# Kernel tuning notes

Measured on AMD Instinct MI355X. Metric: run time of the kernel, lower is better.

The kernel has to match this reference:

```python
import jax, jax.numpy as jnp
import numpy as np

NEG = -9e15  # kept for fidelity though mask is unused in original forward

def setup_inputs() -> dict:
    key = jax.random.key(0)
    k1, k2, k3 = jax.random.split(key, 3)
    N, Fin, Fout = 8192, 512, 256
    x = jax.random.normal(k1, (N, Fin), dtype=jnp.float32)
    # xavier_uniform with gain=1.414 ~ U(-b, b), b = gain*sqrt(6/(fan_in+fan_out))
    bW = 1.414 * np.sqrt(6.0 / (Fin + Fout))
    W = jax.random.uniform(k2, (Fin, Fout), minval=-bW, maxval=bW, dtype=jnp.float32)
    ba = 1.414 * np.sqrt(6.0 / (2 * Fout + 1))
    a = jax.random.uniform(k3, (2 * Fout, 1), minval=-ba, maxval=ba, dtype=jnp.float32)
    return {"x": x, "W": W, "a": a}

def reference(x, W, a):
    # h: [N, Fout]
    h = x @ W
    Fout = h.shape[1]
    # Algebraic decomposition of additive score: e_ij = relu(a1.h_i + a2.h_j)
    a1, a2 = a[:Fout, 0], a[Fout:, 0]  # [Fout], [Fout]
    f = h @ a1  # [N] contribution of row node i
    g = h @ a2  # [N] contribution of col node j
    e = jax.nn.relu(f[:, None] + g[None, :])  # [N, N]
    attention = jax.nn.softmax(e, axis=1)
    h_prime = attention @ h  # [N, Fout]
    return jax.nn.elu(h_prime)
```

## Files before the change

kernel.cpp:

```cpp
#include <hip/hip_runtime.h>
#include <math.h>

#define NROWS 8192
#define FIN   512
#define FOUT  256
#define NCHUNK 512
#define CHROWS 16

typedef _Float16 f16;
typedef _Float16 f16x8 __attribute__((ext_vector_type(8)));
typedef float    f32x4 __attribute__((ext_vector_type(4)));

__global__ __launch_bounds__(256) void prep(const float* __restrict__ x,
                                            const float* __restrict__ W,
                                            f16* __restrict__ xh,
                                            f16* __restrict__ Wt,
                                            float* __restrict__ fg) {
    const int b = blockIdx.x, t = threadIdx.x;
    if (b < 256) {
        const size_t base = (size_t)b * 16384;
#pragma unroll 4
        for (int i = 0; i < 16; ++i) {
            const size_t idx = base + (size_t)i * 1024 + t * 4;
            float4 v = *(const float4*)&x[idx];
            union { f16 h[4]; ushort4 u; } cv;
            cv.h[0] = (f16)v.x; cv.h[1] = (f16)v.y;
            cv.h[2] = (f16)v.z; cv.h[3] = (f16)v.w;
            *(ushort4*)&xh[idx] = cv.u;
        }
    } else {
        const int n = b - 256;
        Wt[(size_t)n * FIN + t]       = (f16)W[(size_t)t * FOUT + n];
        Wt[(size_t)n * FIN + t + 256] = (f16)W[(size_t)(t + 256) * FOUT + n];
        if (n < 64) fg[n * 256 + t] = 0.f;
    }
}

__global__ __launch_bounds__(256) void gemm_fg(const f16* __restrict__ xh,
                                               const f16* __restrict__ Wt,
                                               const float* __restrict__ a,
                                               f16* __restrict__ h,
                                               float* __restrict__ f,
                                               float* __restrict__ g) {
    __shared__ __align__(16) f16 As[64][136];
    __shared__ __align__(16) f16 Bs[64][136];
    __shared__ float sf[2][64], sg[2][64];
    const int tid = threadIdx.x;
    const int n0 = blockIdx.x * 64;
    const int m0 = blockIdx.y * 64;
    const int srow = tid >> 2, sseg = (tid & 3) * 8;
    const int w = tid >> 6, lane = tid & 63;
    const int wm = (w & 1) * 32, wn = (w >> 1) * 32;
    const int l15 = lane & 15, quad = lane >> 4;

    f16x8 pa[4], pb[4];
#pragma unroll
    for (int j = 0; j < 4; ++j) {
        pa[j] = *(const f16x8*)&xh[(size_t)(m0 + srow) * FIN + j * 32 + sseg];
        pb[j] = *(const f16x8*)&Wt[(size_t)(n0 + srow) * FIN + j * 32 + sseg];
    }

    f32x4 acc[2][2] = {};
    for (int k0 = 0; k0 < FIN; k0 += 128) {
        __syncthreads();
#pragma unroll
        for (int j = 0; j < 4; ++j) {
            *(f16x8*)&As[srow][j * 32 + sseg] = pa[j];
            *(f16x8*)&Bs[srow][j * 32 + sseg] = pb[j];
        }
        __syncthreads();
        if (k0 + 128 < FIN) {
#pragma unroll
            for (int j = 0; j < 4; ++j) {
                pa[j] = *(const f16x8*)&xh[(size_t)(m0 + srow) * FIN + k0 + 128 + j * 32 + sseg];
                pb[j] = *(const f16x8*)&Wt[(size_t)(n0 + srow) * FIN + k0 + 128 + j * 32 + sseg];
            }
        }
#pragma unroll
        for (int kk = 0; kk < 4; ++kk) {
            f16x8 af[2], bf[2];
#pragma unroll
            for (int ti = 0; ti < 2; ++ti)
                af[ti] = *(const f16x8*)&As[wm + ti * 16 + l15][kk * 32 + quad * 8];
#pragma unroll
            for (int tj = 0; tj < 2; ++tj)
                bf[tj] = *(const f16x8*)&Bs[wn + tj * 16 + l15][kk * 32 + quad * 8];
#pragma unroll
            for (int ti = 0; ti < 2; ++ti)
#pragma unroll
                for (int tj = 0; tj < 2; ++tj)
                    acc[ti][tj] = __builtin_amdgcn_mfma_f32_16x16x32_f16(af[ti], bf[tj], acc[ti][tj], 0, 0, 0);
        }
    }
#pragma unroll
    for (int ti = 0; ti < 2; ++ti)
#pragma unroll
        for (int tj = 0; tj < 2; ++tj) {
            const int col = n0 + wn + tj * 16 + l15;
#pragma unroll
            for (int r = 0; r < 4; ++r) {
                const int row = m0 + wm + ti * 16 + quad * 4 + r;
                h[(size_t)row * FOUT + col] = (f16)acc[ti][tj][r];
            }
        }
    const float a1c0 = a[n0 + wn + l15];
    const float a1c1 = a[n0 + wn + 16 + l15];
    const float a2c0 = a[FOUT + n0 + wn + l15];
    const float a2c1 = a[FOUT + n0 + wn + 16 + l15];
    const int wnIdx = w >> 1;
#pragma unroll
    for (int ti = 0; ti < 2; ++ti) {
        float pf[4], pg[4];
#pragma unroll
        for (int r = 0; r < 4; ++r) {
            pf[r] = acc[ti][0][r] * a1c0 + acc[ti][1][r] * a1c1;
            pg[r] = acc[ti][0][r] * a2c0 + acc[ti][1][r] * a2c1;
        }
#pragma unroll
        for (int off = 8; off >= 1; off >>= 1)
#pragma unroll
            for (int r = 0; r < 4; ++r) {
                pf[r] += __shfl_xor(pf[r], off, 16);
                pg[r] += __shfl_xor(pg[r], off, 16);
            }
        if (l15 == 0)
#pragma unroll
            for (int r = 0; r < 4; ++r) {
                sf[wnIdx][wm + ti * 16 + quad * 4 + r] = pf[r];
                sg[wnIdx][wm + ti * 16 + quad * 4 + r] = pg[r];
            }
    }
    __syncthreads();
    if (tid < 64) {
        atomicAdd(&f[m0 + tid], sf[0][tid] + sf[1][tid]);
        atomicAdd(&g[m0 + tid], sg[0][tid] + sg[1][tid]);
    }
}

__global__ __launch_bounds__(256) void rank_scatter(const float* __restrict__ g,
                                                    float* __restrict__ gs,
                                                    int* __restrict__ perm) {
    const int t = threadIdx.x;
    const int jl = t & 31;
    const int seg = t >> 5;
    const int j = blockIdx.x * 32 + jl;
    const float gj = g[j];
    const int base = seg * (NROWS / 8);
    int cnt = 0;
    for (int r = 0; r < NROWS / 8; r += 4) {
        const float4 v = *(const float4*)&g[base + r];
        const int i0 = base + r;
        cnt += (v.x < gj) || (v.x == gj && (i0 + 0) < j);
        cnt += (v.y < gj) || (v.y == gj && (i0 + 1) < j);
        cnt += (v.z < gj) || (v.z == gj && (i0 + 2) < j);
        cnt += (v.w < gj) || (v.w == gj && (i0 + 3) < j);
    }
    __shared__ int part[8][32];
    part[seg][jl] = cnt;
    __syncthreads();
    if (seg == 0) {
        int rank = 0;
#pragma unroll
        for (int s = 0; s < 8; ++s) rank += part[s][jl];
        gs[rank] = gj;
        perm[rank] = j;
    }
}

__global__ __launch_bounds__(256) void scan_pass1(const f16* __restrict__ h,
                                                  const int* __restrict__ perm,
                                                  const float* __restrict__ gs,
                                                  const float* __restrict__ f,
                                                  float* __restrict__ c0,
                                                  float* __restrict__ c1,
                                                  float* __restrict__ c1s,
                                                  int* __restrict__ n0arr) {
    const int b = blockIdx.x, c = threadIdx.x;
    if (b < NCHUNK) {
        const int base = b * CHROWS;
        __shared__ int p[CHROWS];
        __shared__ float wl[CHROWS];
        if (c < CHROWS) {
            p[c] = perm[base + c];
            wl[c] = expf(gs[base + c] - gs[NROWS - 1]);
        }
        __syncthreads();
        float s0 = 0.f, s1 = 0.f;
        for (int r = 0; r < CHROWS; ++r) {
            float v = (float)h[(size_t)p[r] * FOUT + c];
            s0 += v;
            s1 += wl[r] * v;
        }
        c0[b * FOUT + c] = s0;
        c1[b * FOUT + c] = s1;
        if (c == 0) {
            float t = 0.f;
            for (int r = 0; r < CHROWS; ++r) t += wl[r];
            c1s[b] = t;
        }
    } else {
        const int i = (b - NCHUNK) * 256 + c;
        const float tt = -f[i];
        int lo = 0, hi = NROWS;
        while (lo < hi) {
            int mid = (lo + hi) >> 1;
            if (gs[mid] <= tt) lo = mid + 1; else hi = mid;
        }
        n0arr[i] = lo;
    }
}

__global__ __launch_bounds__(256) void scan_pass2(const float* __restrict__ c0,
                                                  const float* __restrict__ c1,
                                                  const float* __restrict__ c1s,
                                                  float* __restrict__ o0,
                                                  float* __restrict__ o1,
                                                  float* __restrict__ o1s) {
    const int b = blockIdx.x, t = threadIdx.x;
    __shared__ float sb[256];
    if (b < 256) {
        const float e0 = c0[(2 * t) * FOUT + b];
        const float e1 = c0[(2 * t + 1) * FOUT + b];
        const float local = e0 + e1;
        sb[t] = local;
        __syncthreads();
        for (int off = 1; off < 256; off <<= 1) {
            float add = (t >= off) ? sb[t - off] : 0.f;
            __syncthreads();
            sb[t] += add;
            __syncthreads();
        }
        const float ex = sb[t] - local;
        o0[(2 * t) * FOUT + b] = ex;
        o0[(2 * t + 1) * FOUT + b] = ex + e0;
    } else if (b < 512) {
        const int col = b - 256;
        const float e0 = c1[(2 * t) * FOUT + col];
        const float e1 = c1[(2 * t + 1) * FOUT + col];
        const float local = e0 + e1;
        sb[t] = local;
        __syncthreads();
        for (int off = 1; off < 256; off <<= 1) {
            float add = (t + off < 256) ? sb[t + off] : 0.f;
            __syncthreads();
            sb[t] += add;
            __syncthreads();
        }
        const float exs = sb[t] - local;
        o1[(2 * t) * FOUT + col] = exs + e1;
        o1[(2 * t + 1) * FOUT + col] = exs;
    } else {
        const float e0 = c1s[2 * t];
        const float e1 = c1s[2 * t + 1];
        const float local = e0 + e1;
        sb[t] = local;
        __syncthreads();
        for (int off = 1; off < 256; off <<= 1) {
            float add = (t + off < 256) ? sb[t + off] : 0.f;
            __syncthreads();
            sb[t] += add;
            __syncthreads();
        }
        const float exs = sb[t] - local;
        o1s[2 * t] = exs + e1;
        o1s[2 * t + 1] = exs;
    }
}

__global__ __launch_bounds__(256) void scan_pass3(const f16* __restrict__ h,
                                                  const int* __restrict__ perm,
                                                  const float* __restrict__ gs,
                                                  const float* __restrict__ o0,
                                                  const float* __restrict__ o1,
                                                  const float* __restrict__ o1s,
                                                  f16* __restrict__ P0,
                                                  f16* __restrict__ S1,
                                                  float* __restrict__ S1s) {
    const int k = blockIdx.x, c = threadIdx.x;
    const int base = k * CHROWS;
    __shared__ int p[CHROWS];
    __shared__ float wl[CHROWS];
    if (c < CHROWS) {
        p[c] = perm[base + c];
        wl[c] = expf(gs[base + c] - gs[NROWS - 1]);
    }
    __syncthreads();
    float run0 = o0[k * FOUT + c];
    for (int r = 0; r < CHROWS; ++r) {
        P0[(size_t)(base + r) * FOUT + c] = (f16)run0;
        run0 += (float)h[(size_t)p[r] * FOUT + c];
    }
    float run1 = o1[k * FOUT + c];
    for (int r = CHROWS - 1; r >= 0; --r) {
        run1 += wl[r] * (float)h[(size_t)p[r] * FOUT + c];
        S1[(size_t)(base + r) * FOUT + c] = (f16)run1;
    }
    if (c == 0) {
        float rs = o1s[k];
        for (int r = CHROWS - 1; r >= 0; --r) { rs += wl[r]; S1s[base + r] = rs; }
    }
    if (k == NCHUNK - 1) {
        P0[(size_t)NROWS * FOUT + c] = (f16)run0;
        S1[(size_t)NROWS * FOUT + c] = (f16)0.f;
        if (c == 0) S1s[NROWS] = 0.f;
    }
}

__global__ __launch_bounds__(256) void final_kernel(const float* __restrict__ f,
                                                    const float* __restrict__ gs,
                                                    const int* __restrict__ n0arr,
                                                    const f16* __restrict__ P0,
                                                    const f16* __restrict__ S1,
                                                    const float* __restrict__ S1s,
                                                    float* __restrict__ out) {
    const int b = blockIdx.x, c = threadIdx.x;
    const float gm = gs[NROWS - 1];
#pragma unroll
    for (int rr = 0; rr < 4; ++rr) {
        const int i = b * 4 + rr;
        const float fi = f[i];
        const int n0 = n0arr[i];
        const float m = fmaxf(0.f, fi + gm);
        const float A = expf(-m);
        const float B = expf(fi + gm - m);
        const float denom = A * (float)n0 + B * S1s[n0];
        const float numer = A * (float)P0[(size_t)n0 * FOUT + c]
                          + B * (float)S1[(size_t)n0 * FOUT + c];
        const float v = numer / denom;
        out[(size_t)i * FOUT + c] = v > 0.f ? v : expm1f(v);
    }
}

extern "C" void kernel_launch(void* const* d_in, const int* in_sizes, int n_in,
                              void* d_out, int out_size, void* d_ws, size_t ws_size,
                              hipStream_t stream) {
    (void)in_sizes; (void)n_in; (void)out_size; (void)ws_size;
    const float* x = (const float*)d_in[0];
    const float* W = (const float*)d_in[1];
    const float* a = (const float*)d_in[2];
    float* out = (float*)d_out;

    char* ws = (char*)d_ws;
    size_t off = 0;
    auto alloc = [&](size_t bytes) -> void* {
        void* p = ws + off;
        off += (bytes + 255) & ~(size_t)255;
        return p;
    };
    f16*   xh   = (f16*)alloc((size_t)NROWS * FIN * 2);
    f16*   Wt   = (f16*)alloc((size_t)FOUT * FIN * 2);
    f16*   h    = (f16*)alloc((size_t)NROWS * FOUT * 2);
    f16*   P0   = (f16*)alloc((size_t)(NROWS + 1) * FOUT * 2);
    f16*   S1   = (f16*)alloc((size_t)(NROWS + 1) * FOUT * 2);
    float* fg   = (float*)alloc(2 * NROWS * 4);
    float* f    = fg;
    float* g    = fg + NROWS;
    float* gs   = (float*)alloc(NROWS * 4);
    int*   perm = (int*)alloc(NROWS * 4);
    int*   n0arr= (int*)alloc(NROWS * 4);
    float* c0   = (float*)alloc(NCHUNK * FOUT * 4);
    float* c1   = (float*)alloc(NCHUNK * FOUT * 4);
    float* o0   = (float*)alloc(NCHUNK * FOUT * 4);
    float* o1   = (float*)alloc(NCHUNK * FOUT * 4);
    float* c1s  = (float*)alloc(NCHUNK * 4);
    float* o1s  = (float*)alloc(NCHUNK * 4);
    float* S1s  = (float*)alloc((NROWS + 1) * 4);

    prep<<<512, 256, 0, stream>>>(x, W, xh, Wt, fg);
    gemm_fg<<<dim3(FOUT / 64, NROWS / 64), 256, 0, stream>>>(xh, Wt, a, h, f, g);
    rank_scatter<<<NROWS / 32, 256, 0, stream>>>(g, gs, perm);
    scan_pass1<<<NCHUNK + 32, 256, 0, stream>>>(h, perm, gs, f, c0, c1, c1s, n0arr);
    scan_pass2<<<513, 256, 0, stream>>>(c0, c1, c1s, o0, o1, o1s);
    scan_pass3<<<NCHUNK, 256, 0, stream>>>(h, perm, gs, o0, o1, o1s, P0, S1, S1s);
    final_kernel<<<NROWS / 4, 256, 0, stream>>>(f, gs, n0arr, P0, S1, S1s, out);
}
```

Measured before the change: 135.1 us.

## Fuse seven stage kernels into one persistent kernel with grid barriers

Replaces the seven separate launches (prep, GEMM, rank, three scan passes, final) with a single persistent kernel of 512 blocks that moves between stages through atomic-counter grid barriers. The counter is zeroed by a memset before launch. Each stage's work is remapped to 512 blocks: rank uses 16 columns per block and final handles 16 rows per block. The goal is to remove per-kernel launch gaps and tail effects. The cost is that all 512 blocks must be co-resident for the spin barriers to be safe, and each barrier adds global-atomic latency.

```diff
diff --git a/kernel.cpp b/kernel.cpp
--- a/kernel.cpp
+++ b/kernel.cpp
@@ -6,201 +6,302 @@
 #define FOUT  256
 #define NCHUNK 512
 #define CHROWS 16
+#define NB    512
 
 typedef _Float16 f16;
 typedef _Float16 f16x8 __attribute__((ext_vector_type(8)));
 typedef float    f32x4 __attribute__((ext_vector_type(4)));
 
-__global__ __launch_bounds__(256) void prep(const float* __restrict__ x,
-                                            const float* __restrict__ W,
-                                            f16* __restrict__ xh,
-                                            f16* __restrict__ Wt,
-                                            float* __restrict__ fg) {
-    const int b = blockIdx.x, t = threadIdx.x;
+constexpr size_t AL(size_t v) { return (v + 255) & ~(size_t)255; }
+constexpr size_t SZ_XH  = (size_t)NROWS * FIN * 2;
+constexpr size_t SZ_WT  = (size_t)FOUT * FIN * 2;
+constexpr size_t SZ_H   = (size_t)NROWS * FOUT * 2;
+constexpr size_t SZ_PS  = (size_t)(NROWS + 1) * FOUT * 2;
+constexpr size_t SZ_FG  = (size_t)2 * NROWS * 4;
+constexpr size_t SZ_I   = (size_t)NROWS * 4;
+constexpr size_t SZ_C   = (size_t)NCHUNK * FOUT * 4;
+constexpr size_t SZ_CS  = (size_t)NCHUNK * 4;
+constexpr size_t SZ_S1S = (size_t)(NROWS + 1) * 4;
+
+constexpr size_t OFF_XH   = 0;
+constexpr size_t OFF_WT   = OFF_XH   + AL(SZ_XH);
+constexpr size_t OFF_H    = OFF_WT   + AL(SZ_WT);
+constexpr size_t OFF_P0   = OFF_H    + AL(SZ_H);
+constexpr size_t OFF_S1   = OFF_P0   + AL(SZ_PS);
+constexpr size_t OFF_FG   = OFF_S1   + AL(SZ_PS);
+constexpr size_t OFF_GS   = OFF_FG   + AL(SZ_FG);
+constexpr size_t OFF_PERM = OFF_GS   + AL(SZ_I);
+constexpr size_t OFF_N0   = OFF_PERM + AL(SZ_I);
+constexpr size_t OFF_C0   = OFF_N0   + AL(SZ_I);
+constexpr size_t OFF_C1   = OFF_C0   + AL(SZ_C);
+constexpr size_t OFF_O0   = OFF_C1   + AL(SZ_C);
+constexpr size_t OFF_O1   = OFF_O0   + AL(SZ_C);
+constexpr size_t OFF_C1S  = OFF_O1   + AL(SZ_C);
+constexpr size_t OFF_O1S  = OFF_C1S  + AL(SZ_CS);
+constexpr size_t OFF_S1S  = OFF_O1S  + AL(SZ_CS);
+constexpr size_t OFF_CNT  = OFF_S1S  + AL(SZ_S1S);
+
+union SmemU {
+    struct { f16 As[64][136]; f16 Bs[64][136]; float sf[2][64], sg[2][64]; } g;
+    struct { int part[16][16]; } r;
+    struct { int p[CHROWS]; float wl[CHROWS]; } c;
+    struct { float sb[256]; } s;
+};
+
+__device__ __forceinline__ void gridbar(unsigned* cnt, unsigned target) {
+    __syncthreads();
+    if (threadIdx.x == 0) {
+        __hip_atomic_fetch_add(cnt, 1u, __ATOMIC_ACQ_REL, __HIP_MEMORY_SCOPE_AGENT);
+        while (__hip_atomic_load(cnt, __ATOMIC_ACQUIRE, __HIP_MEMORY_SCOPE_AGENT) < target) {
+        }
+    }
+    __syncthreads();
+}
+
+__global__ __launch_bounds__(256, 2) void mega(const float* __restrict__ x,
+                                               const float* __restrict__ W,
+                                               const float* __restrict__ a,
+                                               float* __restrict__ out,
+                                               char* __restrict__ ws) {
+    __shared__ SmemU sm;
+    const int b = blockIdx.x, tid = threadIdx.x;
+
+    f16*   xh   = (f16*)(ws + OFF_XH);
+    f16*   Wt   = (f16*)(ws + OFF_WT);
+    f16*   hb   = (f16*)(ws + OFF_H);
+    f16*   P0b  = (f16*)(ws + OFF_P0);
+    f16*   S1b  = (f16*)(ws + OFF_S1);
+    float* fArr = (float*)(ws + OFF_FG);
+    float* gArr = fArr + NROWS;
+    float* gs   = (float*)(ws + OFF_GS);
+    int*   perm = (int*)(ws + OFF_PERM);
+    int*   n0arr= (int*)(ws + OFF_N0);
+    float* c0   = (float*)(ws + OFF_C0);
+    float* c1   = (float*)(ws + OFF_C1);
+    float* o0   = (float*)(ws + OFF_O0);
+    float* o1   = (float*)(ws + OFF_O1);
+    float* c1s  = (float*)(ws + OFF_C1S);
+    float* o1s  = (float*)(ws + OFF_O1S);
+    float* S1s  = (float*)(ws + OFF_S1S);
+    unsigned* cnt = (unsigned*)(ws + OFF_CNT);
+
     if (b < 256) {
         const size_t base = (size_t)b * 16384;
 #pragma unroll 4
         for (int i = 0; i < 16; ++i) {
-            const size_t idx = base + (size_t)i * 1024 + t * 4;
+            const size_t idx = base + (size_t)i * 1024 + tid * 4;
             float4 v = *(const float4*)&x[idx];
-            union { f16 h[4]; ushort4 u; } cv;
-            cv.h[0] = (f16)v.x; cv.h[1] = (f16)v.y;
-            cv.h[2] = (f16)v.z; cv.h[3] = (f16)v.w;
+            union { f16 h4[4]; ushort4 u; } cv;
+            cv.h4[0] = (f16)v.x; cv.h4[1] = (f16)v.y;
+            cv.h4[2] = (f16)v.z; cv.h4[3] = (f16)v.w;
             *(ushort4*)&xh[idx] = cv.u;
         }
     } else {
         const int n = b - 256;
-        Wt[(size_t)n * FIN + t]       = (f16)W[(size_t)t * FOUT + n];
-        Wt[(size_t)n * FIN + t + 256] = (f16)W[(size_t)(t + 256) * FOUT + n];
-        if (n < 64) fg[n * 256 + t] = 0.f;
-    }
-}
-
-__global__ __launch_bounds__(256) void gemm_fg(const f16* __restrict__ xh,
-                                               const f16* __restrict__ Wt,
-                                               const float* __restrict__ a,
-                                               f16* __restrict__ h,
-                                               float* __restrict__ f,
-                                               float* __restrict__ g) {
-    __shared__ __align__(16) f16 As[64][136];
-    __shared__ __align__(16) f16 Bs[64][136];
-    __shared__ float sf[2][64], sg[2][64];
-    const int tid = threadIdx.x;
-    const int n0 = blockIdx.x * 64;
-    const int m0 = blockIdx.y * 64;
-    const int srow = tid >> 2, sseg = (tid & 3) * 8;
-    const int w = tid >> 6, lane = tid & 63;
-    const int wm = (w & 1) * 32, wn = (w >> 1) * 32;
-    const int l15 = lane & 15, quad = lane >> 4;
-
-    f16x8 pa[4], pb[4];
-#pragma unroll
-    for (int j = 0; j < 4; ++j) {
-        pa[j] = *(const f16x8*)&xh[(size_t)(m0 + srow) * FIN + j * 32 + sseg];
-        pb[j] = *(const f16x8*)&Wt[(size_t)(n0 + srow) * FIN + j * 32 + sseg];
-    }
-
-    f32x4 acc[2][2] = {};
-    for (int k0 = 0; k0 < FIN; k0 += 128) {
-        __syncthreads();
+        Wt[(size_t)n * FIN + tid]       = (f16)W[(size_t)tid * FOUT + n];
+        Wt[(size_t)n * FIN + tid + 256] = (f16)W[(size_t)(tid + 256) * FOUT + n];
+        if (n < 64) fArr[n * 256 + tid] = 0.f;
+    }
+    gridbar(cnt, 1 * NB);
+
+    {
+        const int n0 = (b & 3) * 64;
+        const int m0 = (b >> 2) * 64;
+        const int srow = tid >> 2, sseg = (tid & 3) * 8;
+        const int w = tid >> 6, lane = tid & 63;
+        const int wm = (w & 1) * 32, wn = (w >> 1) * 32;
+        const int l15 = lane & 15, quad = lane >> 4;
+
+        f16x8 pa[4], pb[4];
 #pragma unroll
         for (int j = 0; j < 4; ++j) {
-            *(f16x8*)&As[srow][j * 32 + sseg] = pa[j];
-            *(f16x8*)&Bs[srow][j * 32 + sseg] = pb[j];
-        }
-        __syncthreads();
-        if (k0 + 128 < FIN) {
+            pa[j] = *(const f16x8*)&xh[(size_t)(m0 + srow) * FIN + j * 32 + sseg];
+            pb[j] = *(const f16x8*)&Wt[(size_t)(n0 + srow) * FIN + j * 32 + sseg];
+        }
+
+        f32x4 acc[2][2] = {};
+        for (int k0 = 0; k0 < FIN; k0 += 128) {
+            __syncthreads();
 #pragma unroll
             for (int j = 0; j < 4; ++j) {
-                pa[j] = *(const f16x8*)&xh[(size_t)(m0 + srow) * FIN + k0 + 128 + j * 32 + sseg];
-                pb[j] = *(const f16x8*)&Wt[(size_t)(n0 + srow) * FIN + k0 + 128 + j * 32 + sseg];
-            }
-        }
-#pragma unroll
-        for (int kk = 0; kk < 4; ++kk) {
-            f16x8 af[2], bf[2];
-#pragma unroll
-            for (int ti = 0; ti < 2; ++ti)
-                af[ti] = *(const f16x8*)&As[wm + ti * 16 + l15][kk * 32 + quad * 8];
-#pragma unroll
-            for (int tj = 0; tj < 2; ++tj)
-                bf[tj] = *(const f16x8*)&Bs[wn + tj * 16 + l15][kk * 32 + quad * 8];
-#pragma unroll
-            for (int ti = 0; ti < 2; ++ti)
+                *(f16x8*)&sm.g.As[srow][j * 32 + sseg] = pa[j];
+                *(f16x8*)&sm.g.Bs[srow][j * 32 + sseg] = pb[j];
+            }
+            __syncthreads();
+            if (k0 + 128 < FIN) {
+#pragma unroll
+                for (int j = 0; j < 4; ++j) {
+                    pa[j] = *(const f16x8*)&xh[(size_t)(m0 + srow) * FIN + k0 + 128 + j * 32 + sseg];
+                    pb[j] = *(const f16x8*)&Wt[(size_t)(n0 + srow) * FIN + k0 + 128 + j * 32 + sseg];
+                }
+            }
+#pragma unroll
+            for (int kk = 0; kk < 4; ++kk) {
+                f16x8 af[2], bf[2];
+#pragma unroll
+                for (int ti = 0; ti < 2; ++ti)
+                    af[ti] = *(const f16x8*)&sm.g.As[wm + ti * 16 + l15][kk * 32 + quad * 8];
 #pragma unroll
                 for (int tj = 0; tj < 2; ++tj)
-                    acc[ti][tj] = __builtin_amdgcn_mfma_f32_16x16x32_f16(af[ti], bf[tj], acc[ti][tj], 0, 0, 0);
-        }
-    }
-#pragma unroll
-    for (int ti = 0; ti < 2; ++ti)
-#pragma unroll
-        for (int tj = 0; tj < 2; ++tj) {
-            const int col = n0 + wn + tj * 16 + l15;
+                    bf[tj] = *(const f16x8*)&sm.g.Bs[wn + tj * 16 + l15][kk * 32 + quad * 8];
+#pragma unroll
+                for (int ti = 0; ti < 2; ++ti)
+#pragma unroll
+                    for (int tj = 0; tj < 2; ++tj)
+                        acc[ti][tj] = __builtin_amdgcn_mfma_f32_16x16x32_f16(af[ti], bf[tj], acc[ti][tj], 0, 0, 0);
+            }
+        }
+#pragma unroll
+        for (int ti = 0; ti < 2; ++ti)
+#pragma unroll
+            for (int tj = 0; tj < 2; ++tj) {
+                const int col = n0 + wn + tj * 16 + l15;
+#pragma unroll
+                for (int r = 0; r < 4; ++r) {
+                    const int row = m0 + wm + ti * 16 + quad * 4 + r;
+                    hb[(size_t)row * FOUT + col] = (f16)acc[ti][tj][r];
+                }
+            }
+        const float a1c0 = a[n0 + wn + l15];
+        const float a1c1 = a[n0 + wn + 16 + l15];
+        const float a2c0 = a[FOUT + n0 + wn + l15];
+        const float a2c1 = a[FOUT + n0 + wn + 16 + l15];
+        const int wnIdx = w >> 1;
+#pragma unroll
+        for (int ti = 0; ti < 2; ++ti) {
+            float pf[4], pg[4];
 #pragma unroll
             for (int r = 0; r < 4; ++r) {
-                const int row = m0 + wm + ti * 16 + quad * 4 + r;
-                h[(size_t)row * FOUT + col] = (f16)acc[ti][tj][r];
-            }
-        }
-    const float a1c0 = a[n0 + wn + l15];
-    const float a1c1 = a[n0 + wn + 16 + l15];
-    const float a2c0 = a[FOUT + n0 + wn + l15];
-    const float a2c1 = a[FOUT + n0 + wn + 16 + l15];
-    const int wnIdx = w >> 1;
-#pragma unroll
-    for (int ti = 0; ti < 2; ++ti) {
-        float pf[4], pg[4];
-#pragma unroll
-        for (int r = 0; r < 4; ++r) {
-            pf[r] = acc[ti][0][r] * a1c0 + acc[ti][1][r] * a1c1;
-            pg[r] = acc[ti][0][r] * a2c0 + acc[ti][1][r] * a2c1;
-        }
-#pragma unroll
-        for (int off = 8; off >= 1; off >>= 1)
-#pragma unroll
-            for (int r = 0; r < 4; ++r) {
-                pf[r] += __shfl_xor(pf[r], off, 16);
-                pg[r] += __shfl_xor(pg[r], off, 16);
-            }
-        if (l15 == 0)
-#pragma unroll
-            for (int r = 0; r < 4; ++r) {
-                sf[wnIdx][wm + ti * 16 + quad * 4 + r] = pf[r];
-                sg[wnIdx][wm + ti * 16 + quad * 4 + r] = pg[r];
-            }
-    }
-    __syncthreads();
-    if (tid < 64) {
-        atomicAdd(&f[m0 + tid], sf[0][tid] + sf[1][tid]);
-        atomicAdd(&g[m0 + tid], sg[0][tid] + sg[1][tid]);
-    }
-}
-
-__global__ __launch_bounds__(256) void rank_scatter(const float* __restrict__ g,
-                                                    float* __restrict__ gs,
-                                                    int* __restrict__ perm) {
-    const int t = threadIdx.x;
-    const int jl = t & 31;
-    const int seg = t >> 5;
-    const int j = blockIdx.x * 32 + jl;
-    const float gj = g[j];
-    const int base = seg * (NROWS / 8);
-    int cnt = 0;
-    for (int r = 0; r < NROWS / 8; r += 4) {
-        const float4 v = *(const float4*)&g[base + r];
-        const int i0 = base + r;
-        cnt += (v.x < gj) || (v.x == gj && (i0 + 0) < j);
-        cnt += (v.y < gj) || (v.y == gj && (i0 + 1) < j);
-        cnt += (v.z < gj) || (v.z == gj && (i0 + 2) < j);
-        cnt += (v.w < gj) || (v.w == gj && (i0 + 3) < j);
-    }
-    __shared__ int part[8][32];
-    part[seg][jl] = cnt;
-    __syncthreads();
-    if (seg == 0) {
-        int rank = 0;
-#pragma unroll
-        for (int s = 0; s < 8; ++s) rank += part[s][jl];
-        gs[rank] = gj;
-        perm[rank] = j;
-    }
-}
-
-__global__ __launch_bounds__(256) void scan_pass1(const f16* __restrict__ h,
-                                                  const int* __restrict__ perm,
-                                                  const float* __restrict__ gs,
-                                                  const float* __restrict__ f,
-                                                  float* __restrict__ c0,
-                                                  float* __restrict__ c1,
-                                                  float* __restrict__ c1s,
-                                                  int* __restrict__ n0arr) {
-    const int b = blockIdx.x, c = threadIdx.x;
-    if (b < NCHUNK) {
+                pf[r] = acc[ti][0][r] * a1c0 + acc[ti][1][r] * a1c1;
+                pg[r] = acc[ti][0][r] * a2c0 + acc[ti][1][r] * a2c1;
+            }
+#pragma unroll
+            for (int off = 8; off >= 1; off >>= 1)
+#pragma unroll
+                for (int r = 0; r < 4; ++r) {
+                    pf[r] += __shfl_xor(pf[r], off, 16);
+                    pg[r] += __shfl_xor(pg[r], off, 16);
+                }
+            if (l15 == 0)
+#pragma unroll
+                for (int r = 0; r < 4; ++r) {
+                    sm.g.sf[wnIdx][wm + ti * 16 + quad * 4 + r] = pf[r];
+                    sm.g.sg[wnIdx][wm + ti * 16 + quad * 4 + r] = pg[r];
+                }
+        }
+        __syncthreads();
+        if (tid < 64) {
+            atomicAdd(&fArr[m0 + tid], sm.g.sf[0][tid] + sm.g.sf[1][tid]);
+            atomicAdd(&gArr[m0 + tid], sm.g.sg[0][tid] + sm.g.sg[1][tid]);
+        }
+    }
+    gridbar(cnt, 2 * NB);
+
+    {
+        const int jl = tid & 15, seg = tid >> 4;
+        const int j = b * 16 + jl;
+        const float gj = gArr[j];
+        const int base = seg * 512;
+        int cntj = 0;
+#pragma unroll 4
+        for (int r = 0; r < 512; r += 4) {
+            const float4 v = *(const float4*)&gArr[base + r];
+            const int i0 = base + r;
+            cntj += (v.x < gj) || (v.x == gj && (i0 + 0) < j);
+            cntj += (v.y < gj) || (v.y == gj && (i0 + 1) < j);
+            cntj += (v.z < gj) || (v.z == gj && (i0 + 2) < j);
+            cntj += (v.w < gj) || (v.w == gj && (i0 + 3) < j);
+        }
+        sm.r.part[seg][jl] = cntj;
+        __syncthreads();
+        if (seg == 0) {
+            int rank = 0;
+#pragma unroll
+            for (int ss = 0; ss < 16; ++ss) rank += sm.r.part[ss][jl];
+            gs[rank] = gj;
+            perm[rank] = j;
+        }
+    }
+    gridbar(cnt, 3 * NB);
+
+    {
         const int base = b * CHROWS;
-        __shared__ int p[CHROWS];
-        __shared__ float wl[CHROWS];
-        if (c < CHROWS) {
-            p[c] = perm[base + c];
-            wl[c] = expf(gs[base + c] - gs[NROWS - 1]);
-        }
-        __syncthreads();
-        float s0 = 0.f, s1 = 0.f;
+        if (tid < CHROWS) {
+            sm.c.p[tid] = perm[base + tid];
+            sm.c.wl[tid] = expf(gs[base + tid] - gs[NROWS - 1]);
+        }
+        __syncthreads();
+        float s0 = 0.f, s1v = 0.f;
         for (int r = 0; r < CHROWS; ++r) {
-            float v = (float)h[(size_t)p[r] * FOUT + c];
+            float v = (float)hb[(size_t)sm.c.p[r] * FOUT + tid];
             s0 += v;
-            s1 += wl[r] * v;
-        }
-        c0[b * FOUT + c] = s0;
-        c1[b * FOUT + c] = s1;
-        if (c == 0) {
-            float t = 0.f;
-            for (int r = 0; r < CHROWS; ++r) t += wl[r];
-            c1s[b] = t;
-        }
-    } else {
-        const int i = (b - NCHUNK) * 256 + c;
-        const float tt = -f[i];
+            s1v += sm.c.wl[r] * v;
+        }
+        c0[b * FOUT + tid] = s0;
+        c1[b * FOUT + tid] = s1v;
+        if (tid == 0) {
+            float t2 = 0.f;
+            for (int r = 0; r < CHROWS; ++r) t2 += sm.c.wl[r];
+            c1s[b] = t2;
+        }
+    }
+    gridbar(cnt, 4 * NB);
+
+    if (b < 256) {
+        const int col = b;
+        {
+            const float e0 = c0[(2 * tid) * FOUT + col];
+            const float e1 = c0[(2 * tid + 1) * FOUT + col];
+            const float local = e0 + e1;
+            sm.s.sb[tid] = local;
+            __syncthreads();
+            for (int off = 1; off < 256; off <<= 1) {
+                float add = (tid >= off) ? sm.s.sb[tid - off] : 0.f;
+                __syncthreads();
+                sm.s.sb[tid] += add;
+                __syncthreads();
+            }
+            const float ex = sm.s.sb[tid] - local;
+            o0[(2 * tid) * FOUT + col] = ex;
+            o0[(2 * tid + 1) * FOUT + col] = ex + e0;
+        }
+        __syncthreads();
+        {
+            const float e0 = c1[(2 * tid) * FOUT + col];
+            const float e1 = c1[(2 * tid + 1) * FOUT + col];
+            const float local = e0 + e1;
+            sm.s.sb[tid] = local;
+            __syncthreads();
+            for (int off = 1; off < 256; off <<= 1) {
+                float add = (tid + off < 256) ? sm.s.sb[tid + off] : 0.f;
+                __syncthreads();
+                sm.s.sb[tid] += add;
+                __syncthreads();
+            }
+            const float exs = sm.s.sb[tid] - local;
+            o1[(2 * tid) * FOUT + col] = exs + e1;
+            o1[(2 * tid + 1) * FOUT + col] = exs;
+        }
+        if (b == 0) {
+            __syncthreads();
+            const float e0 = c1s[2 * tid];
+            const float e1 = c1s[2 * tid + 1];
+            const float local = e0 + e1;
+            sm.s.sb[tid] = local;
+            __syncthreads();
+            for (int off = 1; off < 256; off <<= 1) {
+                float add = (tid + off < 256) ? sm.s.sb[tid + off] : 0.f;
+                __syncthreads();
+                sm.s.sb[tid] += add;
+                __syncthreads();
+            }
+            const float exs = sm.s.sb[tid] - local;
+            o1s[2 * tid] = exs + e1;
+            o1s[2 * tid + 1] = exs;
+        }
+    } else if (b < 288) {
+        const int i = (b - 256) * 256 + tid;
+        const float tt = -fArr[i];
         int lo = 0, hi = NROWS;
         while (lo < hi) {
             int mid = (lo + hi) >> 1;
@@ -208,126 +309,53 @@
         }
         n0arr[i] = lo;
     }
-}
-
-__global__ __launch_bounds__(256) void scan_pass2(const float* __restrict__ c0,
-                                                  const float* __restrict__ c1,
-                                                  const float* __restrict__ c1s,
-                                                  float* __restrict__ o0,
-                                                  float* __restrict__ o1,
-                                                  float* __restrict__ o1s) {
-    const int b = blockIdx.x, t = threadIdx.x;
-    __shared__ float sb[256];
-    if (b < 256) {
-        const float e0 = c0[(2 * t) * FOUT + b];
-        const float e1 = c0[(2 * t + 1) * FOUT + b];
-        const float local = e0 + e1;
-        sb[t] = local;
-        __syncthreads();
-        for (int off = 1; off < 256; off <<= 1) {
-            float add = (t >= off) ? sb[t - off] : 0.f;
-            __syncthreads();
-            sb[t] += add;
-            __syncthreads();
-        }
-        const float ex = sb[t] - local;
-        o0[(2 * t) * FOUT + b] = ex;
-        o0[(2 * t + 1) * FOUT + b] = ex + e0;
-    } else if (b < 512) {
-        const int col = b - 256;
-        const float e0 = c1[(2 * t) * FOUT + col];
-        const float e1 = c1[(2 * t + 1) * FOUT + col];
-        const float local = e0 + e1;
-        sb[t] = local;
-        __syncthreads();
-        for (int off = 1; off < 256; off <<= 1) {
-            float add = (t + off < 256) ? sb[t + off] : 0.f;
-            __syncthreads();
-            sb[t] += add;
-            __syncthreads();
-        }
-        const float exs = sb[t] - local;
-        o1[(2 * t) * FOUT + col] = exs + e1;
-        o1[(2 * t + 1) * FOUT + col] = exs;
-    } else {
-        const float e0 = c1s[2 * t];
-        const float e1 = c1s[2 * t + 1];
-        const float local = e0 + e1;
-        sb[t] = local;
-        __syncthreads();
-        for (int off = 1; off < 256; off <<= 1) {
-            float add = (t + off < 256) ? sb[t + off] : 0.f;
-            __syncthreads();
-            sb[t] += add;
-            __syncthreads();
-        }
-        const float exs = sb[t] - local;
-        o1s[2 * t] = exs + e1;
-        o1s[2 * t + 1] = exs;
-    }
-}
-
-__global__ __launch_bounds__(256) void scan_pass3(const f16* __restrict__ h,
-                                                  const int* __restrict__ perm,
-                                                  const float* __restrict__ gs,
-                                                  const float* __restrict__ o0,
-                                                  const float* __restrict__ o1,
-                                                  const float* __restrict__ o1s,
-                                                  f16* __restrict__ P0,
-                                                  f16* __restrict__ S1,
-                                                  float* __restrict__ S1s) {
-    const int k = blockIdx.x, c = threadIdx.x;
-    const int base = k * CHROWS;
-    __shared__ int p[CHROWS];
-    __shared__ float wl[CHROWS];
-    if (c < CHROWS) {
-        p[c] = perm[base + c];
-        wl[c] = expf(gs[base + c] - gs[NROWS - 1]);
-    }
-    __syncthreads();
-    float run0 = o0[k * FOUT + c];
-    for (int r = 0; r < CHROWS; ++r) {
-        P0[(size_t)(base + r) * FOUT + c] = (f16)run0;
-        run0 += (float)h[(size_t)p[r] * FOUT + c];
-    }
-    float run1 = o1[k * FOUT + c];
-    for (int r = CHROWS - 1; r >= 0; --r) {
-        run1 += wl[r] * (float)h[(size_t)p[r] * FOUT + c];
-        S1[(size_t)(base + r) * FOUT + c] = (f16)run1;
-    }
-    if (c == 0) {
-        float rs = o1s[k];
-        for (int r = CHROWS - 1; r >= 0; --r) { rs += wl[r]; S1s[base + r] = rs; }
-    }
-    if (k == NCHUNK - 1) {
-        P0[(size_t)NROWS * FOUT + c] = (f16)run0;
-        S1[(size_t)NROWS * FOUT + c] = (f16)0.f;
-        if (c == 0) S1s[NROWS] = 0.f;
-    }
-}
-
-__global__ __launch_bounds__(256) void final_kernel(const float* __restrict__ f,
-                                                    const float* __restrict__ gs,
-                                                    const int* __restrict__ n0arr,
-                                                    const f16* __restrict__ P0,
-                                                    const f16* __restrict__ S1,
-                                                    const float* __restrict__ S1s,
-                                                    float* __restrict__ out) {
-    const int b = blockIdx.x, c = threadIdx.x;
-    const float gm = gs[NROWS - 1];
-#pragma unroll
-    for (int rr = 0; rr < 4; ++rr) {
-        const int i = b * 4 + rr;
-        const float fi = f[i];
-        const int n0 = n0arr[i];
-        const float m = fmaxf(0.f, fi + gm);
-        const float A = expf(-m);
-        const float B = expf(fi + gm - m);
-        const float denom = A * (float)n0 + B * S1s[n0];
-        const float numer = A * (float)P0[(size_t)n0 * FOUT + c]
-                          + B * (float)S1[(size_t)n0 * FOUT + c];
-        const float v = numer / denom;
-        out[(size_t)i * FOUT + c] = v > 0.f ? v : expm1f(v);
+    gridbar(cnt, 5 * NB);
+
+    {
+        const int base = b * CHROWS;
+        if (tid < CHROWS) {
+            sm.c.p[tid] = perm[base + tid];
+            sm.c.wl[tid] = expf(gs[base + tid] - gs[NROWS - 1]);
+        }
+        __syncthreads();
+        float run0 = o0[b * FOUT + tid];
+        for (int r = 0; r < CHROWS; ++r) {
+            P0b[(size_t)(base + r) * FOUT + tid] = (f16)run0;
+            run0 += (float)hb[(size_t)sm.c.p[r] * FOUT + tid];
+        }
+        float run1 = o1[b * FOUT + tid];
+        for (int r = CHROWS - 1; r >= 0; --r) {
+            run1 += sm.c.wl[r] * (float)hb[(size_t)sm.c.p[r] * FOUT + tid];
+            S1b[(size_t)(base + r) * FOUT + tid] = (f16)run1;
+        }
+        if (tid == 0) {
+            float rs = o1s[b];
+            for (int r = CHROWS - 1; r >= 0; --r) { rs += sm.c.wl[r]; S1s[base + r] = rs; }
+        }
+        if (b == NCHUNK - 1) {
+            P0b[(size_t)NROWS * FOUT + tid] = (f16)run0;
+            S1b[(size_t)NROWS * FOUT + tid] = (f16)0.f;
+            if (tid == 0) S1s[NROWS] = 0.f;
+        }
+    }
+    gridbar(cnt, 6 * NB);
+
+    {
+        const float gm = gs[NROWS - 1];
+#pragma unroll 4
+        for (int rr = 0; rr < 16; ++rr) {
+            const int i = b * 16 + rr;
+            const float fi = fArr[i];
+            const int n0i = n0arr[i];
+            const float m = fmaxf(0.f, fi + gm);
+            const float A = expf(-m);
+            const float B = expf(fi + gm - m);
+            const float denom = A * (float)n0i + B * S1s[n0i];
+            const float numer = A * (float)P0b[(size_t)n0i * FOUT + tid]
+                              + B * (float)S1b[(size_t)n0i * FOUT + tid];
+            const float v = numer / denom;
+            out[(size_t)i * FOUT + tid] = v > 0.f ? v : expm1f(v);
+        }
     }
 }
 
@@ -339,38 +367,8 @@
     const float* W = (const float*)d_in[1];
     const float* a = (const float*)d_in[2];
     float* out = (float*)d_out;
-
     char* ws = (char*)d_ws;
-    size_t off = 0;
-    auto alloc = [&](size_t bytes) -> void* {
-        void* p = ws + off;
-        off += (bytes + 255) & ~(size_t)255;
-        return p;
-    };
-    f16*   xh   = (f16*)alloc((size_t)NROWS * FIN * 2);
-    f16*   Wt   = (f16*)alloc((size_t)FOUT * FIN * 2);
-    f16*   h    = (f16*)alloc((size_t)NROWS * FOUT * 2);
-    f16*   P0   = (f16*)alloc((size_t)(NROWS + 1) * FOUT * 2);
-    f16*   S1   = (f16*)alloc((size_t)(NROWS + 1) * FOUT * 2);
-    float* fg   = (float*)alloc(2 * NROWS * 4);
-    float* f    = fg;
-    float* g    = fg + NROWS;
-    float* gs   = (float*)alloc(NROWS * 4);
-    int*   perm = (int*)alloc(NROWS * 4);
-    int*   n0arr= (int*)alloc(NROWS * 4);
-    float* c0   = (float*)alloc(NCHUNK * FOUT * 4);
-    float* c1   = (float*)alloc(NCHUNK * FOUT * 4);
-    float* o0   = (float*)alloc(NCHUNK * FOUT * 4);
-    float* o1   = (float*)alloc(NCHUNK * FOUT * 4);
-    float* c1s  = (float*)alloc(NCHUNK * 4);
-    float* o1s  = (float*)alloc(NCHUNK * 4);
-    float* S1s  = (float*)alloc((NROWS + 1) * 4);
-
-    prep<<<512, 256, 0, stream>>>(x, W, xh, Wt, fg);
-    gemm_fg<<<dim3(FOUT / 64, NROWS / 64), 256, 0, stream>>>(xh, Wt, a, h, f, g);
-    rank_scatter<<<NROWS / 32, 256, 0, stream>>>(g, gs, perm);
-    scan_pass1<<<NCHUNK + 32, 256, 0, stream>>>(h, perm, gs, f, c0, c1, c1s, n0arr);
-    scan_pass2<<<513, 256, 0, stream>>>(c0, c1, c1s, o0, o1, o1s);
-    scan_pass3<<<NCHUNK, 256, 0, stream>>>(h, perm, gs, o0, o1, o1s, P0, S1, S1s);
-    final_kernel<<<NROWS / 4, 256, 0, stream>>>(f, gs, n0arr, P0, S1, S1s, out);
+
+    hipMemsetAsync(ws + OFF_CNT, 0, 256, stream);
+    mega<<<NB, 256, 0, stream>>>(x, W, a, out, ws);
 }
```

Measured after the change: 401.4 us. 197% more time.

## Fuse x fp16 conversion into GEMM and fold chunk-prefix scan into pass3

Applied to the files above, without the earlier changes.

Removes the separate x-to-fp16 conversion pass by loading fp32 x tiles in the GEMM and converting them just before the shared-memory store. Also drops the scan_pass2 kernel: each scan_pass3 block now computes its chunk offsets by summing all earlier or later chunk totals directly and reducing c1s in shared memory. This saves a kernel launch, a buffer and the x round-trip, but every scan block now reads the full chunk-total arrays, which is heavily redundant work.

```diff
diff --git a/kernel.cpp b/kernel.cpp
--- a/kernel.cpp
+++ b/kernel.cpp
@@ -11,32 +11,16 @@
 typedef _Float16 f16x8 __attribute__((ext_vector_type(8)));
 typedef float    f32x4 __attribute__((ext_vector_type(4)));
 
-__global__ __launch_bounds__(256) void prep(const float* __restrict__ x,
-                                            const float* __restrict__ W,
-                                            f16* __restrict__ xh,
-                                            f16* __restrict__ Wt,
-                                            float* __restrict__ fg) {
-    const int b = blockIdx.x, t = threadIdx.x;
-    if (b < 256) {
-        const size_t base = (size_t)b * 16384;
-#pragma unroll 4
-        for (int i = 0; i < 16; ++i) {
-            const size_t idx = base + (size_t)i * 1024 + t * 4;
-            float4 v = *(const float4*)&x[idx];
-            union { f16 h[4]; ushort4 u; } cv;
-            cv.h[0] = (f16)v.x; cv.h[1] = (f16)v.y;
-            cv.h[2] = (f16)v.z; cv.h[3] = (f16)v.w;
-            *(ushort4*)&xh[idx] = cv.u;
-        }
-    } else {
-        const int n = b - 256;
-        Wt[(size_t)n * FIN + t]       = (f16)W[(size_t)t * FOUT + n];
-        Wt[(size_t)n * FIN + t + 256] = (f16)W[(size_t)(t + 256) * FOUT + n];
-        if (n < 64) fg[n * 256 + t] = 0.f;
-    }
-}
-
-__global__ __launch_bounds__(256) void gemm_fg(const f16* __restrict__ xh,
+__global__ __launch_bounds__(256) void prep_wt(const float* __restrict__ W,
+                                               f16* __restrict__ Wt,
+                                               float* __restrict__ fg) {
+    const int n = blockIdx.x, t = threadIdx.x;
+    Wt[(size_t)n * FIN + t]       = (f16)W[(size_t)t * FOUT + n];
+    Wt[(size_t)n * FIN + t + 256] = (f16)W[(size_t)(t + 256) * FOUT + n];
+    if (n < 64) fg[n * 256 + t] = 0.f;
+}
+
+__global__ __launch_bounds__(256) void gemm_fg(const float* __restrict__ x,
                                                const f16* __restrict__ Wt,
                                                const float* __restrict__ a,
                                                f16* __restrict__ h,
@@ -53,10 +37,13 @@
     const int wm = (w & 1) * 32, wn = (w >> 1) * 32;
     const int l15 = lane & 15, quad = lane >> 4;
 
-    f16x8 pa[4], pb[4];
+    float4 pa0[4], pa1[4];
+    f16x8 pb[4];
 #pragma unroll
     for (int j = 0; j < 4; ++j) {
-        pa[j] = *(const f16x8*)&xh[(size_t)(m0 + srow) * FIN + j * 32 + sseg];
+        const float* xp = &x[(size_t)(m0 + srow) * FIN + j * 32 + sseg];
+        pa0[j] = *(const float4*)xp;
+        pa1[j] = *(const float4*)(xp + 4);
         pb[j] = *(const f16x8*)&Wt[(size_t)(n0 + srow) * FIN + j * 32 + sseg];
     }
 
@@ -65,14 +52,21 @@
         __syncthreads();
 #pragma unroll
         for (int j = 0; j < 4; ++j) {
-            *(f16x8*)&As[srow][j * 32 + sseg] = pa[j];
+            f16x8 t;
+            t[0] = (f16)pa0[j].x; t[1] = (f16)pa0[j].y;
+            t[2] = (f16)pa0[j].z; t[3] = (f16)pa0[j].w;
+            t[4] = (f16)pa1[j].x; t[5] = (f16)pa1[j].y;
+            t[6] = (f16)pa1[j].z; t[7] = (f16)pa1[j].w;
+            *(f16x8*)&As[srow][j * 32 + sseg] = t;
             *(f16x8*)&Bs[srow][j * 32 + sseg] = pb[j];
         }
         __syncthreads();
         if (k0 + 128 < FIN) {
 #pragma unroll
             for (int j = 0; j < 4; ++j) {
-                pa[j] = *(const f16x8*)&xh[(size_t)(m0 + srow) * FIN + k0 + 128 + j * 32 + sseg];
+                const float* xp = &x[(size_t)(m0 + srow) * FIN + k0 + 128 + j * 32 + sseg];
+                pa0[j] = *(const float4*)xp;
+                pa1[j] = *(const float4*)(xp + 4);
                 pb[j] = *(const f16x8*)&Wt[(size_t)(n0 + srow) * FIN + k0 + 128 + j * 32 + sseg];
             }
         }
@@ -210,69 +204,12 @@
     }
 }
 
-__global__ __launch_bounds__(256) void scan_pass2(const float* __restrict__ c0,
-                                                  const float* __restrict__ c1,
-                                                  const float* __restrict__ c1s,
-                                                  float* __restrict__ o0,
-                                                  float* __restrict__ o1,
-                                                  float* __restrict__ o1s) {
-    const int b = blockIdx.x, t = threadIdx.x;
-    __shared__ float sb[256];
-    if (b < 256) {
-        const float e0 = c0[(2 * t) * FOUT + b];
-        const float e1 = c0[(2 * t + 1) * FOUT + b];
-        const float local = e0 + e1;
-        sb[t] = local;
-        __syncthreads();
-        for (int off = 1; off < 256; off <<= 1) {
-            float add = (t >= off) ? sb[t - off] : 0.f;
-            __syncthreads();
-            sb[t] += add;
-            __syncthreads();
-        }
-        const float ex = sb[t] - local;
-        o0[(2 * t) * FOUT + b] = ex;
-        o0[(2 * t + 1) * FOUT + b] = ex + e0;
-    } else if (b < 512) {
-        const int col = b - 256;
-        const float e0 = c1[(2 * t) * FOUT + col];
-        const float e1 = c1[(2 * t + 1) * FOUT + col];
-        const float local = e0 + e1;
-        sb[t] = local;
-        __syncthreads();
-        for (int off = 1; off < 256; off <<= 1) {
-            float add = (t + off < 256) ? sb[t + off] : 0.f;
-            __syncthreads();
-            sb[t] += add;
-            __syncthreads();
-        }
-        const float exs = sb[t] - local;
-        o1[(2 * t) * FOUT + col] = exs + e1;
-        o1[(2 * t + 1) * FOUT + col] = exs;
-    } else {
-        const float e0 = c1s[2 * t];
-        const float e1 = c1s[2 * t + 1];
-        const float local = e0 + e1;
-        sb[t] = local;
-        __syncthreads();
-        for (int off = 1; off < 256; off <<= 1) {
-            float add = (t + off < 256) ? sb[t + off] : 0.f;
-            __syncthreads();
-            sb[t] += add;
-            __syncthreads();
-        }
-        const float exs = sb[t] - local;
-        o1s[2 * t] = exs + e1;
-        o1s[2 * t + 1] = exs;
-    }
-}
-
 __global__ __launch_bounds__(256) void scan_pass3(const f16* __restrict__ h,
                                                   const int* __restrict__ perm,
                                                   const float* __restrict__ gs,
-                                                  const float* __restrict__ o0,
-                                                  const float* __restrict__ o1,
-                                                  const float* __restrict__ o1s,
+                                                  const float* __restrict__ c0,
+                                                  const float* __restrict__ c1,
+                                                  const float* __restrict__ c1s,
                                                   f16* __restrict__ P0,
                                                   f16* __restrict__ S1,
                                                   float* __restrict__ S1s) {
@@ -280,23 +217,39 @@
     const int base = k * CHROWS;
     __shared__ int p[CHROWS];
     __shared__ float wl[CHROWS];
+    __shared__ float red[256];
     if (c < CHROWS) {
         p[c] = perm[base + c];
         wl[c] = expf(gs[base + c] - gs[NROWS - 1]);
     }
+    float s0 = 0.f, s1 = 0.f;
+#pragma unroll 4
+    for (int j = 0; j < NCHUNK; ++j) {
+        const float v0 = c0[j * FOUT + c];
+        const float v1 = c1[j * FOUT + c];
+        s0 += (j < k) ? v0 : 0.f;
+        s1 += (j > k) ? v1 : 0.f;
+    }
+    red[c] = ((c > k) ? c1s[c] : 0.f) + ((c + 256 > k) ? c1s[c + 256] : 0.f);
     __syncthreads();
-    float run0 = o0[k * FOUT + c];
+    for (int off = 128; off >= 1; off >>= 1) {
+        if (c < off) red[c] += red[c + off];
+        __syncthreads();
+    }
+    const float o1sk = red[0];
+
+    float run0 = s0;
     for (int r = 0; r < CHROWS; ++r) {
         P0[(size_t)(base + r) * FOUT + c] = (f16)run0;
         run0 += (float)h[(size_t)p[r] * FOUT + c];
     }
-    float run1 = o1[k * FOUT + c];
+    float run1 = s1;
     for (int r = CHROWS - 1; r >= 0; --r) {
         run1 += wl[r] * (float)h[(size_t)p[r] * FOUT + c];
         S1[(size_t)(base + r) * FOUT + c] = (f16)run1;
     }
     if (c == 0) {
-        float rs = o1s[k];
+        float rs = o1sk;
         for (int r = CHROWS - 1; r >= 0; --r) { rs += wl[r]; S1s[base + r] = rs; }
     }
     if (k == NCHUNK - 1) {
@@ -347,7 +300,6 @@
         off += (bytes + 255) & ~(size_t)255;
         return p;
     };
-    f16*   xh   = (f16*)alloc((size_t)NROWS * FIN * 2);
     f16*   Wt   = (f16*)alloc((size_t)FOUT * FIN * 2);
     f16*   h    = (f16*)alloc((size_t)NROWS * FOUT * 2);
     f16*   P0   = (f16*)alloc((size_t)(NROWS + 1) * FOUT * 2);
@@ -360,17 +312,13 @@
     int*   n0arr= (int*)alloc(NROWS * 4);
     float* c0   = (float*)alloc(NCHUNK * FOUT * 4);
     float* c1   = (float*)alloc(NCHUNK * FOUT * 4);
-    float* o0   = (float*)alloc(NCHUNK * FOUT * 4);
-    float* o1   = (float*)alloc(NCHUNK * FOUT * 4);
     float* c1s  = (float*)alloc(NCHUNK * 4);
-    float* o1s  = (float*)alloc(NCHUNK * 4);
     float* S1s  = (float*)alloc((NROWS + 1) * 4);
 
-    prep<<<512, 256, 0, stream>>>(x, W, xh, Wt, fg);
-    gemm_fg<<<dim3(FOUT / 64, NROWS / 64), 256, 0, stream>>>(xh, Wt, a, h, f, g);
+    prep_wt<<<256, 256, 0, stream>>>(W, Wt, fg);
+    gemm_fg<<<dim3(FOUT / 64, NROWS / 64), 256, 0, stream>>>(x, Wt, a, h, f, g);
     rank_scatter<<<NROWS / 32, 256, 0, stream>>>(g, gs, perm);
     scan_pass1<<<NCHUNK + 32, 256, 0, stream>>>(h, perm, gs, f, c0, c1, c1s, n0arr);
-    scan_pass2<<<513, 256, 0, stream>>>(c0, c1, c1s, o0, o1, o1s);
-    scan_pass3<<<NCHUNK, 256, 0, stream>>>(h, perm, gs, o0, o1, o1s, P0, S1, S1s);
+    scan_pass3<<<NCHUNK, 256, 0, stream>>>(h, perm, gs, c0, c1, c1s, P0, S1, S1s);
     final_kernel<<<NROWS / 4, 256, 0, stream>>>(f, gs, n0arr, P0, S1, S1s, out);
 }
```

Measured after the change: 172.3 us. +27.5%, slower.
